# Optimization experiments

Hardware: AMD Instinct MI355X
Metric: run time of the kernel (lower is better)

Reference implementation:

```python
import jax, jax.numpy as jnp
import numpy as np

L, N, E, D, H, B = 4, 50000, 800000, 128, 64, 16384
ED = 2 * D  # edge_dim
K = 7      # conv1d kernel size


def setup_inputs() -> dict:
    key = jax.random.key(0)
    ks = jax.random.split(key, 12)
    return {
        "x_nodes": jax.random.normal(ks[0], (L, N, 1), jnp.float32),
        "edge_index": jax.random.randint(ks[1], (L, 2, E), 0, N),
        "W1": jax.random.normal(ks[2], (L, 1, H), jnp.float32) * 0.1,
        "b1": jnp.zeros((L, H), jnp.float32),
        "gamma": jnp.ones((L, H), jnp.float32),
        "beta": jnp.zeros((L, H), jnp.float32),
        "W2": jax.random.normal(ks[3], (L, H, D), jnp.float32) * 0.05,
        "b2": jnp.zeros((L, D), jnp.float32),
        "conv_w": jax.random.normal(ks[4], (ED, ED, K), jnp.float32) * 0.02,
        "conv_b": jnp.zeros((ED,), jnp.float32),
        "lc_w": jax.random.normal(ks[5], (ED, L), jnp.float32) * 0.05,
        "lc_b": jnp.zeros((L,), jnp.float32),
        "link_w": jax.random.normal(ks[6], (ED, 2), jnp.float32) * 0.05,
        "link_b": jnp.zeros((2,), jnp.float32),
        "now_layer": jax.random.randint(ks[7], (B,), 0, L),
        "leftnode": jax.random.randint(ks[8], (B,), 0, N),
        "rightnode": jax.random.randint(ks[9], (B,), 0, N),
    }


def gcn_conv(x, src, dst, norm, W, b):
    # x: [N, Fin] -> [N, Fout]; symmetric-normalized message passing (GCNConv)
    xw = x @ W
    out = jax.ops.segment_sum(norm[:, None] * xw[src], dst, num_segments=N)
    return out + b


def gcn_layer(x, ei, W1, b1, g, bt, W2, b2):
    loops = jnp.arange(N, dtype=ei.dtype)
    src = jnp.concatenate([ei[0], loops])
    dst = jnp.concatenate([ei[1], loops])
    deg = jax.ops.segment_sum(jnp.ones_like(src, jnp.float32), dst, num_segments=N)
    dis = jax.lax.rsqrt(jnp.maximum(deg, 1e-12))
    norm = dis[src] * dis[dst]
    h = gcn_conv(x, src, dst, norm, W1, b1)
    # BatchNorm1d (training mode: batch stats over nodes)
    mu = h.mean(axis=0)
    var = h.var(axis=0)
    h = g * (h - mu) * jax.lax.rsqrt(var + 1e-5) + bt
    h = jax.nn.relu(h)
    return gcn_conv(h, src, dst, norm, W2, b2)


def reference(x_nodes, edge_index, W1, b1, gamma, beta, W2, b2,
              conv_w, conv_b, lc_w, lc_b, link_w, link_b,
              now_layer, leftnode, rightnode):
    # Per-layer GCN embeddings (fixed small L -> Python loop is fine, keeps peak memory low)
    embeds = jnp.stack([
        gcn_layer(x_nodes[i], edge_index[i], W1[i], b1[i], gamma[i], beta[i], W2[i], b2[i])
        for i in range(L)
    ])  # [L, N, D]

    # Edge features: gather per-sample layer-specific node embeddings and concat
    left = embeds[now_layer, leftnode]    # [B, D]
    right = embeds[now_layer, rightnode]  # [B, D]
    layer_specific = jnp.concatenate([left, right], axis=-1)  # [B, ED]

    # Conv1d applied unbatched on [ED, B] (convolves across batch dim, as in original)
    dn = jax.lax.conv_dimension_numbers((1, ED, B), (ED, ED, K), ('NCH', 'OIH', 'NCH'))
    y = jax.lax.conv_general_dilated(layer_specific.T[None], conv_w, (1,), [(3, 3)],
                                     dimension_numbers=dn)[0]  # [ED, B]
    shared = jax.nn.relu(y + conv_b[:, None]).T  # [B, ED]

    discriminant_outs = shared @ lc_w + lc_b  # [B, L]

    # Ortho_algorithm: remove shared component from specific, combine with shared
    dot = jnp.sum(layer_specific * shared, axis=-1, keepdims=True)
    nrm = jnp.sum(shared * shared, axis=-1, keepdims=True)
    enhanced = layer_specific - (dot / (nrm + 1e-12)) * shared + shared  # [B, ED]

    prediction_outs = enhanced @ link_w + link_b  # [B, 2]
    return prediction_outs, discriminant_outs
```

## Files before the change

### kernel.cpp

```cpp
#include <hip/hip_runtime.h>
#include <hip/hip_bf16.h>

#define Lc 4
#define Nc 50000
#define Ec 800000
#define Bc 16384
#define EDc 256
#define Kc 7
#define Mtot (Lc * Nc)
#define KDIM (EDc * Kc)

#define BINW 512
#define FB 98
#define NBINS (FB * Lc)
#define CAPc 12288
#define CHUNK 8192

typedef __attribute__((ext_vector_type(8))) short bf16x8;
typedef __attribute__((ext_vector_type(4))) float f32x4;

static __device__ __forceinline__ unsigned short f2bf(float f) {
    unsigned u = __float_as_uint(f);
    unsigned r = (u + 0x7fffu + ((u >> 16) & 1u)) >> 16;
    return (unsigned short)r;
}


__global__ void k_binfill(const int* __restrict__ ei, int* __restrict__ binCursor,
                          int* __restrict__ binned) {
    int l = blockIdx.y;
    int e0 = blockIdx.x * CHUNK;
    __shared__ int lh[FB], lcur[FB];
    if (threadIdx.x < FB) lh[threadIdx.x] = 0;
    __syncthreads();
    const int* srcp = ei + (size_t)l * 2 * Ec;
    const int* dstp = srcp + Ec;
#pragma unroll
    for (int it = 0; it < CHUNK / 256; it++) {
        int idx = e0 + it * 256 + threadIdx.x;
        if (idx < Ec) atomicAdd(&lh[dstp[idx] >> 9], 1);
    }
    __syncthreads();
    if (threadIdx.x < FB) {
        int c = lh[threadIdx.x];
        int bin = l * FB + threadIdx.x;
        int st = c ? atomicAdd(&binCursor[bin], c) : 0;
        lcur[threadIdx.x] = bin * CAPc + min(st, CAPc);
        lh[threadIdx.x] = bin * CAPc + CAPc;
    }
    __syncthreads();
#pragma unroll
    for (int it = 0; it < CHUNK / 256; it++) {
        int idx = e0 + it * 256 + threadIdx.x;
        if (idx < Ec) {
            int d = dstp[idx], sv = srcp[idx];
            int t = d >> 9;
            int pos = atomicAdd(&lcur[t], 1);
            if (pos < lh[t]) binned[pos] = (sv << 9) | (d & (BINW - 1));
        }
    }
}

__global__ __launch_bounds__(512) void k_csr(const int* __restrict__ binCnt,
                                             const int* __restrict__ binned,
                                             const float* __restrict__ x_nodes,
                                             int* __restrict__ csr,
                                             int* __restrict__ rstart,
                                             int* __restrict__ cnt,
                                             float* __restrict__ dis,
                                             float* __restrict__ g) {
    int b = blockIdx.x;
    int l = b / FB, gg = b % FB;
    int rs = b * CAPc;
    int cntb = binCnt[b];
    if (cntb > CAPc) cntb = CAPc;
    int re = rs + cntb;
    __shared__ int hist[BINW];
    hist[threadIdx.x] = 0;
    __syncthreads();
    for (int i = rs + threadIdx.x; i < re; i += 512)
        atomicAdd(&hist[binned[i] & (BINW - 1)], 1);
    __syncthreads();
    int lane = threadIdx.x & 63, wid = threadIdx.x >> 6;
    int v = hist[threadIdx.x];
    int x = v;
#pragma unroll
    for (int off = 1; off < 64; off <<= 1) {
        int y = __shfl_up(x, off);
        if (lane >= off) x += y;
    }
    __shared__ int ws[8];
    if (lane == 63) ws[wid] = x;
    __syncthreads();
    int carry = 0;
    for (int w = 0; w < wid; w++) carry += ws[w];
    int exc = x - v + carry;
    int n = gg * BINW + threadIdx.x;
    int n4 = l * Nc + n;
    if (n < Nc) {
        rstart[n4] = rs + exc;
        cnt[n4] = v;
        float dn = rsqrtf((float)v + 1.0f);
        dis[n4] = dn;
        g[n4] = dn * x_nodes[(size_t)l * Nc + n];
    }
    __syncthreads();
    hist[threadIdx.x] = rs + exc;
    __syncthreads();
    for (int i = rs + threadIdx.x; i < re; i += 512) {
        unsigned p = (unsigned)binned[i];
        int pos = atomicAdd(&hist[p & (BINW - 1)], 1);
        csr[pos] = (int)(p >> 9);
    }
}


__global__ __launch_bounds__(512) void k_s_bin(const int* __restrict__ binCnt,
                                               const int* __restrict__ binned,
                                               const float* __restrict__ g,
                                               const float* __restrict__ dis,
                                               float* __restrict__ s,
                                               double* __restrict__ stats) {
    int b = blockIdx.x;
    int l = b / FB, gg = b % FB;
    int rs = b * CAPc;
    int cntb = binCnt[b];
    if (cntb > CAPc) cntb = CAPc;
    int re = rs + cntb;
    const float* gl = g + (size_t)l * Nc;
    __shared__ float acc[BINW];
    acc[threadIdx.x] = 0.f;
    __syncthreads();
    for (int i = rs + threadIdx.x; i < re; i += 512) {
        unsigned p = (unsigned)binned[i];
        atomicAdd(&acc[p & (BINW - 1)], gl[p >> 9]);
    }
    __syncthreads();
    int n = gg * BINW + threadIdx.x;
    int n4 = l * Nc + n;
    double v = 0.0, v2 = 0.0;
    if (n < Nc) {
        float dn = dis[n4];
        float sf = dn * (acc[threadIdx.x] + g[n4]);
        s[n4] = sf;
        v = (double)sf;
        v2 = (double)sf * (double)sf;
    }
    for (int m = 32; m; m >>= 1) { v += __shfl_xor(v, m); v2 += __shfl_xor(v2, m); }
    __shared__ double r0[8], r1[8];
    int wid = threadIdx.x >> 6, lane = threadIdx.x & 63;
    if (lane == 0) { r0[wid] = v; r1[wid] = v2; }
    __syncthreads();
    if (threadIdx.x == 0) {
        double a = 0, bb = 0;
        for (int w = 0; w < 8; w++) { a += r0[w]; bb += r1[w]; }
        atomicAdd(&stats[l * 2 + 0], a);
        atomicAdd(&stats[l * 2 + 1], bb);
    }
}

__global__ void k_cvec4(const double* __restrict__ stats, const float* __restrict__ W1,
                        const float* __restrict__ gamma, float* __restrict__ cbuf) {
    int l = threadIdx.x >> 6, h = threadIdx.x & 63;
    double mean = stats[l * 2] / (double)Nc;
    double var = stats[l * 2 + 1] / (double)Nc - mean * mean;
    float w = W1[l * 64 + h];
    cbuf[l * 72 + h] = gamma[l * 64 + h] * w * rsqrtf((float)var * w * w + 1e-5f);
    if (h == 0) cbuf[l * 72 + 64] = (float)mean;
}


__global__ __launch_bounds__(128) void k_embed4(const int* __restrict__ now,
        const int* __restrict__ lnn, const int* __restrict__ rnn,
        const int* __restrict__ row_start, const int* __restrict__ cnt,
        const int* __restrict__ csr, const float* __restrict__ dis,
        const float* __restrict__ s, const float* __restrict__ cbuf,
        const float* __restrict__ beta, const float* __restrict__ W2,
        const float* __restrict__ b2, float* __restrict__ lsb,
        unsigned short* __restrict__ lsbh) {
    int b = blockIdx.x;
    int l = now[b];
    int side = threadIdx.x >> 6, lane = threadIdx.x & 63;
    int n = side ? rnn[b] : lnn[b];
    int n4 = l * Nc + n;
    float c = cbuf[l * 72 + lane], mu = cbuf[l * 72 + 64], bt = beta[l * 64 + lane];
    const float* dl = dis + (size_t)l * Nc;
    const float* sl = s + (size_t)l * Nc;
    int st = row_start[n4], deg = cnt[n4];
    float a = 0.f;
    for (int base = 0; base < deg; base += 64) {
        int e = base + lane;
        int sv = (e < deg) ? csr[st + e] : 0;
        float nv = (e < deg) ? dl[sv] : 0.f;
        float fv = (e < deg) ? sl[sv] : 0.f;
        int m = min(64, deg - base);
        for (int j = 0; j < m; j++) {
            float nj = __shfl(nv, j);
            float fj = __shfl(fv, j);
            float hv = fmaxf(c * (fj - mu) + bt, 0.f);
            a += nj * hv;
        }
    }
    float dn = dl[n];
    float hself = fmaxf(c * (sl[n] - mu) + bt, 0.f);
    a = dn * a + dn * dn * hself;
    const float* W2l = W2 + (size_t)l * 64 * 128;
    const float* b2l = b2 + (size_t)l * 128;
    float o0 = b2l[lane], o1 = b2l[lane + 64];
    for (int hh = 0; hh < 64; hh++) {
        float ah = __shfl(a, hh);
        o0 += ah * W2l[hh * 128 + lane];
        o1 += ah * W2l[hh * 128 + lane + 64];
    }
    size_t obase = (size_t)b * 256 + side * 128;
    lsb[obase + lane] = o0;
    lsb[obase + lane + 64] = o1;
    lsbh[obase + lane] = f2bf(o0);
    lsbh[obase + lane + 64] = f2bf(o1);
}


__global__ void k_wbf(const float* __restrict__ w, unsigned short* __restrict__ wbt) {
    int i = blockIdx.x * 256 + threadIdx.x;
    int co = i / KDIM;
    int r = i % KDIM;
    int ci = r / Kc, k = r % Kc;
    wbt[(size_t)co * KDIM + k * EDc + ci] = f2bf(w[i]);
}

__global__ __launch_bounds__(512, 1) void k_convmma(const unsigned short* __restrict__ lsbh,
                                                    const unsigned short* __restrict__ wbt,
                                                    const float* __restrict__ cb,
                                                    float* __restrict__ sh) {
    __shared__ unsigned short lsa[70 * EDc];
    int b0 = blockIdx.x * 64;
    int wid = threadIdx.x >> 6, lane = threadIdx.x & 63;
    int lrow = lane & 15, lg = lane >> 4;

    for (int idx = threadIdx.x; idx < 70 * 32; idx += 512) {
        int r = idx >> 5, c = idx & 31;
        int grow = b0 - 3 + r;
        uint4 v = make_uint4(0u, 0u, 0u, 0u);
        if ((unsigned)grow < (unsigned)Bc)
            v = *(const uint4*)(lsbh + (size_t)grow * EDc + c * 8);
        int byte = (r * 512 + c * 16) ^ ((r & 7) << 4);
        *(uint4*)((char*)lsa + byte) = v;
    }
    __syncthreads();

    const unsigned short* w0 = wbt + (size_t)(wid * 32 + lrow) * KDIM + lg * 8;

    f32x4 acc[4][2] = {};
    bf16x8 br0[8][2], br1[8][2];

#pragma unroll
    for (int tt = 0; tt < 8; tt++)
#pragma unroll
        for (int ni = 0; ni < 2; ni++)
            br0[tt][ni] = *(const bf16x8*)(w0 + ni * 16 * KDIM + tt * 32);

#pragma unroll
    for (int k = 0; k < Kc; k++) {
        if (k < Kc - 1) {
#pragma unroll
            for (int tt = 0; tt < 8; tt++)
#pragma unroll
                for (int ni = 0; ni < 2; ni++) {
                    bf16x8 v = *(const bf16x8*)(w0 + ni * 16 * KDIM + (k + 1) * 256 + tt * 32);
                    if (k & 1) br0[tt][ni] = v; else br1[tt][ni] = v;
                }
        }
#pragma unroll
        for (int tt = 0; tt < 8; tt++) {
            bf16x8 a[4];
#pragma unroll
            for (int mi = 0; mi < 4; mi++) {
                int l = mi * 16 + lrow + k;
                a[mi] = *(const bf16x8*)((const char*)lsa + l * 512
                        + ((lg * 16 + tt * 64) ^ ((l & 7) << 4)));
            }
#pragma unroll
            for (int mi = 0; mi < 4; mi++)
#pragma unroll
                for (int ni = 0; ni < 2; ni++) {
                    bf16x8 bv = (k & 1) ? br1[tt][ni] : br0[tt][ni];
                    acc[mi][ni] = __builtin_amdgcn_mfma_f32_16x16x32_bf16(
                        a[mi], bv, acc[mi][ni], 0, 0, 0);
                }
        }
    }

#pragma unroll
    for (int mi = 0; mi < 4; mi++) {
        int rbase = b0 + mi * 16 + lg * 4;
#pragma unroll
        for (int ni = 0; ni < 2; ni++) {
            int co = wid * 32 + ni * 16 + lrow;
            float bias = cb[co];
#pragma unroll
            for (int r = 0; r < 4; r++)
                sh[(size_t)(rbase + r) * EDc + co] = fmaxf(acc[mi][ni][r] + bias, 0.0f);
        }
    }
}

__global__ void k_final(const float* __restrict__ ls, const float* __restrict__ sh,
                        const float* __restrict__ lc_w, const float* __restrict__ lc_b,
                        const float* __restrict__ link_w, const float* __restrict__ link_b,
                        float* __restrict__ out) {
    int b = blockIdx.x, lane = threadIdx.x;
    float lsv[4], shv[4];
    float dot = 0.f, nrm = 0.f;
#pragma unroll
    for (int i = 0; i < 4; i++) {
        int ci = lane + i * 64;
        lsv[i] = ls[b * 256 + ci];
        shv[i] = sh[b * 256 + ci];
        dot += lsv[i] * shv[i];
        nrm += shv[i] * shv[i];
    }
    for (int m = 32; m; m >>= 1) { dot += __shfl_xor(dot, m); nrm += __shfl_xor(nrm, m); }
    float coef = dot / (nrm + 1e-12f);
    float p0 = 0.f, p1 = 0.f, d0 = 0.f, d1 = 0.f, d2 = 0.f, d3 = 0.f;
#pragma unroll
    for (int i = 0; i < 4; i++) {
        int ci = lane + i * 64;
        float e = lsv[i] - coef * shv[i] + shv[i];
        p0 += e * link_w[ci * 2];
        p1 += e * link_w[ci * 2 + 1];
        d0 += shv[i] * lc_w[ci * 4];
        d1 += shv[i] * lc_w[ci * 4 + 1];
        d2 += shv[i] * lc_w[ci * 4 + 2];
        d3 += shv[i] * lc_w[ci * 4 + 3];
    }
    for (int m = 32; m; m >>= 1) {
        p0 += __shfl_xor(p0, m); p1 += __shfl_xor(p1, m);
        d0 += __shfl_xor(d0, m); d1 += __shfl_xor(d1, m);
        d2 += __shfl_xor(d2, m); d3 += __shfl_xor(d3, m);
    }
    if (lane == 0) {
        out[b * 2]     = p0 + link_b[0];
        out[b * 2 + 1] = p1 + link_b[1];
        float* dd = out + 2 * Bc;
        dd[b * 4]     = d0 + lc_b[0];
        dd[b * 4 + 1] = d1 + lc_b[1];
        dd[b * 4 + 2] = d2 + lc_b[2];
        dd[b * 4 + 3] = d3 + lc_b[3];
    }
}


extern "C" void kernel_launch(void* const* d_in, const int* in_sizes, int n_in,
                              void* d_out, int out_size, void* d_ws, size_t ws_size,
                              hipStream_t stream) {
    const float* x_nodes    = (const float*)d_in[0];
    const int*   edge_index = (const int*)d_in[1];
    const float* W1   = (const float*)d_in[2];
    const float* gamma = (const float*)d_in[4];
    const float* beta  = (const float*)d_in[5];
    const float* W2   = (const float*)d_in[6];
    const float* b2   = (const float*)d_in[7];
    const float* conv_w = (const float*)d_in[8];
    const float* conv_b = (const float*)d_in[9];
    const float* lc_w   = (const float*)d_in[10];
    const float* lc_b   = (const float*)d_in[11];
    const float* link_w = (const float*)d_in[12];
    const float* link_b = (const float*)d_in[13];
    const int* now = (const int*)d_in[14];
    const int* ln  = (const int*)d_in[15];
    const int* rn  = (const int*)d_in[16];
    float* out = (float*)d_out;

    char* base = (char*)d_ws;
    size_t off = 0;
    auto carve = [&](size_t bytes) {
        void* p = base + off;
        off = (off + bytes + 255) & ~(size_t)255;
        return p;
    };
    int*    binCursor = (int*)carve(NBINS * 4);
    double* stats     = (double*)carve(8 * 8);
    int*    binned    = (int*)carve((size_t)NBINS * CAPc * 4);
    int*    rstart    = (int*)carve((size_t)Mtot * 4);
    int*    cnt       = (int*)carve((size_t)Mtot * 4);
    int*    csr       = (int*)carve((size_t)NBINS * CAPc * 4);
    float*  dis       = (float*)carve((size_t)Mtot * 4);
    float*  s         = (float*)carve((size_t)Mtot * 4);
    float*  g         = (float*)carve((size_t)Mtot * 4);
    float*  cbuf      = (float*)carve(Lc * 72 * 4);
    float*  lsb       = (float*)carve((size_t)Bc * 256 * 4);
    float*  shb       = (float*)carve((size_t)Bc * 256 * 4);
    unsigned short* lsbh = (unsigned short*)carve((size_t)Bc * 256 * 2);
    unsigned short* wbt  = (unsigned short*)carve((size_t)EDc * KDIM * 2);
    (void)ws_size;

    const int FBLK = (Ec + CHUNK - 1) / CHUNK;

    hipMemsetAsync(binCursor, 0, (char*)(stats + 8) - (char*)binCursor, stream);
    k_wbf<<<1792, 256, 0, stream>>>(conv_w, wbt);

    k_binfill<<<dim3(FBLK, Lc), 256, 0, stream>>>(edge_index, binCursor, binned);
    k_csr<<<NBINS, 512, 0, stream>>>(binCursor, binned, x_nodes, csr, rstart, cnt, dis, g);
    k_s_bin<<<NBINS, 512, 0, stream>>>(binCursor, binned, g, dis, s, stats);
    k_cvec4<<<1, 256, 0, stream>>>(stats, W1, gamma, cbuf);
    k_embed4<<<Bc, 128, 0, stream>>>(now, ln, rn, rstart, cnt, csr, dis, s,
                                     cbuf, beta, W2, b2, lsb, lsbh);

    k_convmma<<<Bc / 64, 512, 0, stream>>>(lsbh, wbt, conv_b, shb);
    k_final<<<Bc, 64, 0, stream>>>(lsb, shb, lc_w, lc_b, link_w, link_b, out);
}
```

Baseline: 185.3 us.

## Build CSR only for queried nodes and batch W2 projection via MFMA

Marks the queried (layer, node) pairs in a bitmap so the CSR scatter writes only edges whose destination is needed. Queries are sorted by layer into padded segments, so neighbour aggregation and the W2 projection can run as separate kernels, the latter as a bf16 MFMA GEMM. Degree norm and s are packed into one float2 to halve gathers, and the bins are shrunk to 256 nodes. The layer-specific features kept for the final step are now bf16 rather than fp32, which adds rounding error, and the change adds several small launch and ordering kernels.

```diff
diff --git a/kernel.cpp b/kernel.cpp
--- a/kernel.cpp
+++ b/kernel.cpp
@@ -10,11 +10,16 @@
 #define Mtot (Lc * Nc)
 #define KDIM (EDc * Kc)
 
-#define BINW 512
-#define FB 98
+#define BINW 256
+#define BSH 8
+#define FB 196
 #define NBINS (FB * Lc)
-#define CAPc 12288
-#define CHUNK 8192
+#define CAPc 6144
+#define CHUNK 2048
+#define FBLK ((Ec + CHUNK - 1) / CHUNK)
+
+#define PADTOT 33024
+#define PADBIT (1 << 24)
 
 typedef __attribute__((ext_vector_type(8))) short bf16x8;
 typedef __attribute__((ext_vector_type(4))) float f32x4;
@@ -23,6 +28,9 @@
     unsigned u = __float_as_uint(f);
     unsigned r = (u + 0x7fffu + ((u >> 16) & 1u)) >> 16;
     return (unsigned short)r;
+}
+static __device__ __forceinline__ float bf2f(unsigned short u) {
+    return __uint_as_float(((unsigned)u) << 16);
 }
 
 
@@ -38,7 +46,7 @@
 #pragma unroll
     for (int it = 0; it < CHUNK / 256; it++) {
         int idx = e0 + it * 256 + threadIdx.x;
-        if (idx < Ec) atomicAdd(&lh[dstp[idx] >> 9], 1);
+        if (idx < Ec) atomicAdd(&lh[dstp[idx] >> BSH], 1);
     }
     __syncthreads();
     if (threadIdx.x < FB) {
@@ -54,9 +62,51 @@
         int idx = e0 + it * 256 + threadIdx.x;
         if (idx < Ec) {
             int d = dstp[idx], sv = srcp[idx];
-            int t = d >> 9;
+            int t = d >> BSH;
             int pos = atomicAdd(&lcur[t], 1);
-            if (pos < lh[t]) binned[pos] = (sv << 9) | (d & (BINW - 1));
+            if (pos < lh[t]) binned[pos] = (sv << BSH) | (d & (BINW - 1));
+        }
+    }
+}
+
+__global__ void k_mark(const int* __restrict__ now, const int* __restrict__ lnn,
+                       const int* __restrict__ rnn, int* __restrict__ ord,
+                       unsigned* __restrict__ bitmap, int* __restrict__ gcnt) {
+    int b = blockIdx.x * 256 + threadIdx.x;
+    for (int p = b; p < PADTOT; p += 16384) ord[p] = PADBIT;
+    int l = now[b];
+    int a1 = l * Nc + lnn[b];
+    atomicOr(&bitmap[a1 >> 5], 1u << (a1 & 31));
+    int a2 = l * Nc + rnn[b];
+    atomicOr(&bitmap[a2 >> 5], 1u << (a2 & 31));
+    int lane = threadIdx.x & 63;
+#pragma unroll
+    for (int ll = 0; ll < 4; ll++) {
+        unsigned long long m = __ballot(l == ll);
+        if (m && lane == __builtin_ctzll(m)) atomicAdd(&gcnt[ll], __popcll(m));
+    }
+}
+
+__global__ void k_order2(const int* __restrict__ now, const int* __restrict__ gcnt,
+                         int* __restrict__ gcur, int* __restrict__ ord) {
+    int b = blockIdx.x * 256 + threadIdx.x;
+    int l = now[b];
+    int segBase = 0;
+    for (int ll = 0; ll < l; ll++) segBase += (2 * gcnt[ll] + 63) & ~63;
+    int lane = threadIdx.x & 63;
+#pragma unroll
+    for (int ll = 0; ll < 4; ll++) {
+        unsigned long long m = __ballot(l == ll);
+        if (!m) continue;
+        int ldr = __builtin_ctzll(m);
+        int bs = 0;
+        if (lane == ldr) bs = atomicAdd(&gcur[ll], __popcll(m));
+        bs = __shfl(bs, ldr);
+        if (l == ll) {
+            int rk = __popcll(m & (lane ? ((1ull << lane) - 1) : 0ull));
+            int sp = segBase + 2 * (bs + rk);
+            ord[sp] = (2 * b) | (ll << 20);
+            ord[sp + 1] = (2 * b + 1) | (ll << 20);
         }
     }
 }
@@ -64,6 +114,7 @@
 __global__ __launch_bounds__(512) void k_csr(const int* __restrict__ binCnt,
                                              const int* __restrict__ binned,
                                              const float* __restrict__ x_nodes,
+                                             const unsigned* __restrict__ bitmap,
                                              int* __restrict__ csr,
                                              int* __restrict__ rstart,
                                              int* __restrict__ cnt,
@@ -76,13 +127,13 @@
     if (cntb > CAPc) cntb = CAPc;
     int re = rs + cntb;
     __shared__ int hist[BINW];
-    hist[threadIdx.x] = 0;
+    if (threadIdx.x < BINW) hist[threadIdx.x] = 0;
     __syncthreads();
     for (int i = rs + threadIdx.x; i < re; i += 512)
         atomicAdd(&hist[binned[i] & (BINW - 1)], 1);
     __syncthreads();
     int lane = threadIdx.x & 63, wid = threadIdx.x >> 6;
-    int v = hist[threadIdx.x];
+    int v = (threadIdx.x < BINW) ? hist[threadIdx.x] : 0;
     int x = v;
 #pragma unroll
     for (int off = 1; off < 64; off <<= 1) {
@@ -93,11 +144,11 @@
     if (lane == 63) ws[wid] = x;
     __syncthreads();
     int carry = 0;
-    for (int w = 0; w < wid; w++) carry += ws[w];
+    for (int w = 0; w < wid && w < 4; w++) carry += ws[w];
     int exc = x - v + carry;
-    int n = gg * BINW + threadIdx.x;
+    int n = gg * BINW + (threadIdx.x & (BINW - 1));
     int n4 = l * Nc + n;
-    if (n < Nc) {
+    if (threadIdx.x < BINW && n < Nc) {
         rstart[n4] = rs + exc;
         cnt[n4] = v;
         float dn = rsqrtf((float)v + 1.0f);
@@ -105,21 +156,25 @@
         g[n4] = dn * x_nodes[(size_t)l * Nc + n];
     }
     __syncthreads();
-    hist[threadIdx.x] = rs + exc;
-    __syncthreads();
+    if (threadIdx.x < BINW) hist[threadIdx.x] = rs + exc;
+    __syncthreads();
+    int lbase = l * Nc + gg * BINW;
     for (int i = rs + threadIdx.x; i < re; i += 512) {
         unsigned p = (unsigned)binned[i];
-        int pos = atomicAdd(&hist[p & (BINW - 1)], 1);
-        csr[pos] = (int)(p >> 9);
-    }
-}
-
+        int d = p & (BINW - 1);
+        int nn4 = lbase + d;
+        if ((bitmap[nn4 >> 5] >> (nn4 & 31)) & 1u) {
+            int pos = atomicAdd(&hist[d], 1);
+            csr[pos] = (int)(p >> BSH);
+        }
+    }
+}
 
 __global__ __launch_bounds__(512) void k_s_bin(const int* __restrict__ binCnt,
                                                const int* __restrict__ binned,
                                                const float* __restrict__ g,
                                                const float* __restrict__ dis,
-                                               float* __restrict__ s,
+                                               float2* __restrict__ ns,
                                                double* __restrict__ stats) {
     int b = blockIdx.x;
     int l = b / FB, gg = b % FB;
@@ -129,20 +184,20 @@
     int re = rs + cntb;
     const float* gl = g + (size_t)l * Nc;
     __shared__ float acc[BINW];
-    acc[threadIdx.x] = 0.f;
+    if (threadIdx.x < BINW) acc[threadIdx.x] = 0.f;
     __syncthreads();
     for (int i = rs + threadIdx.x; i < re; i += 512) {
         unsigned p = (unsigned)binned[i];
-        atomicAdd(&acc[p & (BINW - 1)], gl[p >> 9]);
-    }
-    __syncthreads();
-    int n = gg * BINW + threadIdx.x;
+        atomicAdd(&acc[p & (BINW - 1)], gl[p >> BSH]);
+    }
+    __syncthreads();
+    int n = gg * BINW + (threadIdx.x & (BINW - 1));
     int n4 = l * Nc + n;
     double v = 0.0, v2 = 0.0;
-    if (n < Nc) {
+    if (threadIdx.x < BINW && n < Nc) {
         float dn = dis[n4];
         float sf = dn * (acc[threadIdx.x] + g[n4]);
-        s[n4] = sf;
+        ns[n4] = make_float2(dn, sf);
         v = (double)sf;
         v2 = (double)sf * (double)sf;
     }
@@ -170,53 +225,67 @@
 }
 
 
-__global__ __launch_bounds__(128) void k_embed4(const int* __restrict__ now,
+__global__ __launch_bounds__(256) void k_agg(const int* __restrict__ ord,
         const int* __restrict__ lnn, const int* __restrict__ rnn,
-        const int* __restrict__ row_start, const int* __restrict__ cnt,
-        const int* __restrict__ csr, const float* __restrict__ dis,
-        const float* __restrict__ s, const float* __restrict__ cbuf,
-        const float* __restrict__ beta, const float* __restrict__ W2,
-        const float* __restrict__ b2, float* __restrict__ lsb,
-        unsigned short* __restrict__ lsbh) {
-    int b = blockIdx.x;
-    int l = now[b];
-    int side = threadIdx.x >> 6, lane = threadIdx.x & 63;
-    int n = side ? rnn[b] : lnn[b];
+        const int* __restrict__ rstart, const int* __restrict__ cnt,
+        const int* __restrict__ csr, const float2* __restrict__ ns,
+        const float* __restrict__ cbuf, const float* __restrict__ beta,
+        unsigned short* __restrict__ acch) {
+    int pos = blockIdx.x * 4 + (threadIdx.x >> 6);
+    int lane = threadIdx.x & 63;
+    int ordv = ord[pos];
+    if (ordv & PADBIT) { acch[(size_t)pos * 64 + lane] = 0; return; }
+    int side = ordv & 0xFFFFF;
+    int l = (ordv >> 20) & 3;
+    int b = side >> 1;
+    int n = (side & 1) ? rnn[b] : lnn[b];
     int n4 = l * Nc + n;
     float c = cbuf[l * 72 + lane], mu = cbuf[l * 72 + 64], bt = beta[l * 64 + lane];
-    const float* dl = dis + (size_t)l * Nc;
-    const float* sl = s + (size_t)l * Nc;
-    int st = row_start[n4], deg = cnt[n4];
+    const float2* nsl = ns + (size_t)l * Nc;
+    int st = rstart[n4], deg = cnt[n4];
     float a = 0.f;
-    for (int base = 0; base < deg; base += 64) {
-        int e = base + lane;
-        int sv = (e < deg) ? csr[st + e] : 0;
-        float nv = (e < deg) ? dl[sv] : 0.f;
-        float fv = (e < deg) ? sl[sv] : 0.f;
-        int m = min(64, deg - base);
-        for (int j = 0; j < m; j++) {
-            float nj = __shfl(nv, j);
-            float fj = __shfl(fv, j);
-            float hv = fmaxf(c * (fj - mu) + bt, 0.f);
-            a += nj * hv;
-        }
-    }
-    float dn = dl[n];
-    float hself = fmaxf(c * (sl[n] - mu) + bt, 0.f);
-    a = dn * a + dn * dn * hself;
-    const float* W2l = W2 + (size_t)l * 64 * 128;
-    const float* b2l = b2 + (size_t)l * 128;
-    float o0 = b2l[lane], o1 = b2l[lane + 64];
-    for (int hh = 0; hh < 64; hh++) {
-        float ah = __shfl(a, hh);
-        o0 += ah * W2l[hh * 128 + lane];
-        o1 += ah * W2l[hh * 128 + lane + 64];
-    }
-    size_t obase = (size_t)b * 256 + side * 128;
-    lsb[obase + lane] = o0;
-    lsb[obase + lane + 64] = o1;
-    lsbh[obase + lane] = f2bf(o0);
-    lsbh[obase + lane + 64] = f2bf(o1);
+    for (int e = 0; e < deg; e++) {
+        int sv = csr[st + e];
+        float2 nf = nsl[sv];
+        a += nf.x * fmaxf(c * (nf.y - mu) + bt, 0.f);
+    }
+    float2 nself = ns[n4];
+    float hs = fmaxf(c * (nself.y - mu) + bt, 0.f);
+    a = nself.x * a + nself.x * nself.x * hs;
+    acch[(size_t)pos * 64 + lane] = f2bf(a);
+}
+
+__global__ __launch_bounds__(256) void k_embgemm(const unsigned short* __restrict__ acch,
+        const int* __restrict__ ord, const unsigned short* __restrict__ w2t,
+        const float* __restrict__ b2, unsigned short* __restrict__ lsh) {
+    int t0 = blockIdx.x * 16;
+    int wn = threadIdx.x >> 6, lane = threadIdx.x & 63;
+    int lrow = lane & 15, lg = lane >> 4;
+    int l = (ord[t0] >> 20) & 3;
+    const unsigned short* ap = acch + (size_t)(t0 + lrow) * 64 + lg * 8;
+    const unsigned short* bp = w2t + (size_t)(l * 128 + wn * 32 + lrow) * 64 + lg * 8;
+    f32x4 acc[2] = {};
+#pragma unroll
+    for (int kt = 0; kt < 2; kt++) {
+        bf16x8 a = *(const bf16x8*)(ap + kt * 32);
+        bf16x8 b0 = *(const bf16x8*)(bp + kt * 32);
+        bf16x8 b1 = *(const bf16x8*)(bp + 16 * 64 + kt * 32);
+        acc[0] = __builtin_amdgcn_mfma_f32_16x16x32_bf16(a, b0, acc[0], 0, 0, 0);
+        acc[1] = __builtin_amdgcn_mfma_f32_16x16x32_bf16(a, b1, acc[1], 0, 0, 0);
+    }
+#pragma unroll
+    for (int r = 0; r < 4; r++) {
+        int pos = t0 + lg * 4 + r;
+        int ordv = ord[pos];
+        if (ordv & PADBIT) continue;
+        int side = ordv & 0xFFFFF;
+        size_t base = (size_t)(side >> 1) * 256 + (side & 1) * 128;
+#pragma unroll
+        for (int ni = 0; ni < 2; ni++) {
+            int n = wn * 32 + ni * 16 + lrow;
+            lsh[base + n] = f2bf(acc[ni][r] + b2[l * 128 + n]);
+        }
+    }
 }
 
 
@@ -228,7 +297,14 @@
     wbt[(size_t)co * KDIM + k * EDc + ci] = f2bf(w[i]);
 }
 
-__global__ __launch_bounds__(512, 1) void k_convmma(const unsigned short* __restrict__ lsbh,
+__global__ void k_w2t(const float* __restrict__ W2, unsigned short* __restrict__ w2t) {
+    int i = blockIdx.x * 256 + threadIdx.x;
+    int l = i >> 13, r = i & 8191;
+    int d = r >> 6, h = r & 63;
+    w2t[i] = f2bf(W2[(size_t)(l * 64 + h) * 128 + d]);
+}
+
+__global__ __launch_bounds__(512, 1) void k_convmma(const unsigned short* __restrict__ lsh,
                                                     const unsigned short* __restrict__ wbt,
                                                     const float* __restrict__ cb,
                                                     float* __restrict__ sh) {
@@ -242,7 +318,7 @@
         int grow = b0 - 3 + r;
         uint4 v = make_uint4(0u, 0u, 0u, 0u);
         if ((unsigned)grow < (unsigned)Bc)
-            v = *(const uint4*)(lsbh + (size_t)grow * EDc + c * 8);
+            v = *(const uint4*)(lsh + (size_t)grow * EDc + c * 8);
         int byte = (r * 512 + c * 16) ^ ((r & 7) << 4);
         *(uint4*)((char*)lsa + byte) = v;
     }
@@ -304,7 +380,7 @@
     }
 }
 
-__global__ void k_final(const float* __restrict__ ls, const float* __restrict__ sh,
+__global__ void k_final(const unsigned short* __restrict__ lsh, const float* __restrict__ sh,
                         const float* __restrict__ lc_w, const float* __restrict__ lc_b,
                         const float* __restrict__ link_w, const float* __restrict__ link_b,
                         float* __restrict__ out) {
@@ -314,7 +390,7 @@
 #pragma unroll
     for (int i = 0; i < 4; i++) {
         int ci = lane + i * 64;
-        lsv[i] = ls[b * 256 + ci];
+        lsv[i] = bf2f(lsh[b * 256 + ci]);
         shv[i] = sh[b * 256 + ci];
         dot += lsv[i] * shv[i];
         nrm += shv[i] * shv[i];
@@ -378,34 +454,42 @@
         off = (off + bytes + 255) & ~(size_t)255;
         return p;
     };
-    int*    binCursor = (int*)carve(NBINS * 4);
-    double* stats     = (double*)carve(8 * 8);
+    int*      binCursor = (int*)carve(NBINS * 4);
+    int*      gcnt      = (int*)carve(4 * 4);
+    int*      gcur      = (int*)carve(4 * 4);
+    unsigned* bitmap    = (unsigned*)carve(6272 * 4);
+    double*   stats     = (double*)carve(8 * 8);
     int*    binned    = (int*)carve((size_t)NBINS * CAPc * 4);
     int*    rstart    = (int*)carve((size_t)Mtot * 4);
     int*    cnt       = (int*)carve((size_t)Mtot * 4);
     int*    csr       = (int*)carve((size_t)NBINS * CAPc * 4);
     float*  dis       = (float*)carve((size_t)Mtot * 4);
-    float*  s         = (float*)carve((size_t)Mtot * 4);
     float*  g         = (float*)carve((size_t)Mtot * 4);
+    float2* ns        = (float2*)carve((size_t)Mtot * 8);
     float*  cbuf      = (float*)carve(Lc * 72 * 4);
-    float*  lsb       = (float*)carve((size_t)Bc * 256 * 4);
+    int*    ord       = (int*)carve((size_t)PADTOT * 4);
+    unsigned short* acch = (unsigned short*)carve((size_t)PADTOT * 64 * 2);
     float*  shb       = (float*)carve((size_t)Bc * 256 * 4);
-    unsigned short* lsbh = (unsigned short*)carve((size_t)Bc * 256 * 2);
-    unsigned short* wbt  = (unsigned short*)carve((size_t)EDc * KDIM * 2);
+    unsigned short* lsh = (unsigned short*)carve((size_t)Bc * 256 * 2);
+    unsigned short* wbt = (unsigned short*)carve((size_t)EDc * KDIM * 2);
+    unsigned short* w2t = (unsigned short*)carve((size_t)Lc * 128 * 64 * 2);
     (void)ws_size;
-
-    const int FBLK = (Ec + CHUNK - 1) / CHUNK;
 
     hipMemsetAsync(binCursor, 0, (char*)(stats + 8) - (char*)binCursor, stream);
     k_wbf<<<1792, 256, 0, stream>>>(conv_w, wbt);
+    k_w2t<<<128, 256, 0, stream>>>(W2, w2t);
+    k_mark<<<64, 256, 0, stream>>>(now, ln, rn, ord, bitmap, gcnt);
 
     k_binfill<<<dim3(FBLK, Lc), 256, 0, stream>>>(edge_index, binCursor, binned);
-    k_csr<<<NBINS, 512, 0, stream>>>(binCursor, binned, x_nodes, csr, rstart, cnt, dis, g);
-    k_s_bin<<<NBINS, 512, 0, stream>>>(binCursor, binned, g, dis, s, stats);
+    k_csr<<<NBINS, 512, 0, stream>>>(binCursor, binned, x_nodes, bitmap,
+                                     csr, rstart, cnt, dis, g);
+    k_s_bin<<<NBINS, 512, 0, stream>>>(binCursor, binned, g, dis, ns, stats);
     k_cvec4<<<1, 256, 0, stream>>>(stats, W1, gamma, cbuf);
-    k_embed4<<<Bc, 128, 0, stream>>>(now, ln, rn, rstart, cnt, csr, dis, s,
-                                     cbuf, beta, W2, b2, lsb, lsbh);
-
-    k_convmma<<<Bc / 64, 512, 0, stream>>>(lsbh, wbt, conv_b, shb);
-    k_final<<<Bc, 64, 0, stream>>>(lsb, shb, lc_w, lc_b, link_w, link_b, out);
-}
+    k_order2<<<64, 256, 0, stream>>>(now, gcnt, gcur, ord);
+    k_agg<<<PADTOT / 4, 256, 0, stream>>>(ord, ln, rn, rstart, cnt, csr, ns,
+                                          cbuf, beta, acch);
+    k_embgemm<<<PADTOT / 16, 256, 0, stream>>>(acch, ord, w2t, b2, lsh);
+
+    k_convmma<<<Bc / 64, 512, 0, stream>>>(lsh, wbt, conv_b, shb);
+    k_final<<<Bc, 64, 0, stream>>>(lsh, shb, lc_w, lc_b, link_w, link_b, out);
+}
```

After: 238.9 us. 28.9% more time.
